# Optimization experiments

Measured on AMD Instinct MI355X. Metric: run time of the kernel, lower is better.

The kernel has to match this reference:

```python
import jax, jax.numpy as jnp
import numpy as np

N = 98304        # total nodes (= 16384 graphs * act_dim 6)
E = 1572864      # edges (avg degree 16)
C = 64           # in_channels
H = 32           # hidden_size
ACT = 6          # act_dim


def setup_inputs() -> dict:
    key = jax.random.key(0)
    ks = jax.random.split(key, 11)
    s = lambda fan: 1.0 / np.sqrt(fan)
    return {
        "state": jax.random.normal(ks[0], (N, C), jnp.float32),
        "edge_index": jax.random.randint(ks[1], (2, E), 0, N, dtype=jnp.int64),
        "conv_W": jax.random.normal(ks[2], (C, C), jnp.float32) * s(C),
        "conv_b": jax.random.normal(ks[3], (C,), jnp.float32) * 0.01,
        "W1": jax.random.normal(ks[4], (C, H), jnp.float32) * s(C),
        "b1": jax.random.normal(ks[5], (H,), jnp.float32) * 0.01,
        "W2": jax.random.normal(ks[6], (H, H), jnp.float32) * s(H),
        "b2": jax.random.normal(ks[7], (H,), jnp.float32) * 0.01,
        "W3": jax.random.normal(ks[8], (H, 1), jnp.float32) * s(H),
        "b3": jax.random.normal(ks[9], (1,), jnp.float32) * 0.01,
    }


def gcn_conv(x, edge_index, W, b):
    # PyG GCNConv: add self-loops, symmetric normalization D^-1/2 (A+I) D^-1/2 (X W) + b
    loops = jnp.arange(N, dtype=edge_index.dtype)
    src = jnp.concatenate([edge_index[0], loops])  # [E+N]
    dst = jnp.concatenate([edge_index[1], loops])  # [E+N]
    deg = jax.ops.segment_sum(jnp.ones(E + N, x.dtype), dst, num_segments=N)
    dinv = jax.lax.rsqrt(deg)                      # deg >= 1 due to self-loops
    norm = dinv[src] * dinv[dst]                   # [E+N]
    h = x @ W                                      # [N, C]
    msg = h[src] * norm[:, None]                   # gather + scale
    return jax.ops.segment_sum(msg, dst, num_segments=N) + b


def reference(state, edge_index, conv_W, conv_b, W1, b1, W2, b2, W3, b3):
    out = jax.nn.relu(gcn_conv(state, edge_index, conv_W, conv_b))
    x = out + state                                # residual
    x = x.reshape(-1, ACT, C)                      # [num_graphs, act_dim, C]
    x = jax.nn.relu(x @ W1 + b1)
    x = jax.nn.relu(x @ W2 + b2)
    x = jax.nn.softplus(x @ W3 + b3)
    concentration = x.squeeze(-1) + 1e-20          # [num_graphs, act_dim]
    return concentration
```

## Files before the change

### kernel.cpp

```cpp
#include <hip/hip_runtime.h>
#include <math.h>

#define Nn 98304
#define Ee 1572864
#define Cc 64
#define Hh 32
#define TT 128
#define NT (Nn / TT)
#define HB 256
#define EPB (Ee / HB)
#define CAPT 2560


__device__ __forceinline__ int detect64(const void* ei) {
    const unsigned int* u = (const unsigned int*)ei;
    int is64 = 1;
    #pragma unroll
    for (int i = 0; i < 16; ++i) is64 &= (u[2 * i + 1] == 0u);
    return is64;
}

__device__ __forceinline__ int load_idx(const void* ei, long e, int is64) {
    if (is64) return (int)((const long long*)ei)[e];
    return ((const int*)ei)[e];
}

__device__ __forceinline__ unsigned short f2bf(float x) {
    union { float f; unsigned int u; } v; v.f = x;
    unsigned int r = v.u + 0x7FFFu + ((v.u >> 16) & 1u);
    return (unsigned short)(r >> 16);
}
__device__ __forceinline__ float bf2f(unsigned short h) {
    union { unsigned int u; float f; } v; v.u = ((unsigned int)h) << 16;
    return v.f;
}

__global__ __launch_bounds__(1024) void k_bucket(const void* __restrict__ ei,
                                                 unsigned int* __restrict__ aux,
                                                 unsigned int* __restrict__ ebuf) {
    __shared__ unsigned int hl[NT];
    __shared__ unsigned int off[NT];
    int t = threadIdx.x, b = blockIdx.x;
    if (t < NT) hl[t] = 0;
    __syncthreads();
    int is64 = detect64(ei);
    long e0 = (long)b * EPB;
    #pragma unroll
    for (int i = 0; i < EPB / 1024; ++i) {
        int d = load_idx(ei, (long)Ee + e0 + i * 1024 + t, is64);
        atomicAdd(&hl[d >> 7], 1u);
    }
    __syncthreads();
    if (t < NT) off[t] = hl[t];
    __syncthreads();
    for (int s = 1; s < NT; s <<= 1) {
        unsigned int v = (t < NT && t >= s) ? off[t - s] : 0u;
        __syncthreads();
        if (t < NT) off[t] += v;
        __syncthreads();
    }
    if (t < NT) {
        unsigned int ex = off[t] - hl[t];
        aux[(long)b * NT + t] = ex | (hl[t] << 16);
        off[t] = ex;
    }
    __syncthreads();
    #pragma unroll
    for (int i = 0; i < EPB / 1024; ++i) {
        long e = e0 + i * 1024 + t;
        int s = load_idx(ei, e, is64);
        int d = load_idx(ei, (long)Ee + e, is64);
        unsigned int pos = atomicAdd(&off[d >> 7], 1u);
        ebuf[(long)b * EPB + pos] = (unsigned int)s | ((unsigned int)(d & (TT - 1)) << 17);
    }
}

__global__ __launch_bounds__(256) void k_nodecnt(const unsigned int* __restrict__ aux,
                                                 const unsigned int* __restrict__ ebuf,
                                                 unsigned int* __restrict__ rowOff,
                                                 unsigned int* __restrict__ rowEnd,
                                                 float* __restrict__ dinv,
                                                 unsigned int* __restrict__ srcs) {
    __shared__ unsigned int stage[CAPT];
    __shared__ unsigned int rbI[HB];
    __shared__ unsigned int ro[HB];
    __shared__ unsigned int cnt[TT];
    __shared__ unsigned int sc[TT];
    __shared__ unsigned int cur[TT];
    int t = threadIdx.x, tile = blockIdx.x;
    if (t < HB) {
        unsigned int av = aux[(long)t * NT + tile];
        ro[t] = av & 0xFFFFu;
        rbI[t] = av >> 16;
    }
    __syncthreads();
    for (int s = 1; s < HB; s <<= 1) {
        unsigned int v = (t < HB && t >= s) ? rbI[t - s] : 0u;
        __syncthreads();
        if (t < HB) rbI[t] += v;
        __syncthreads();
    }
    int total = (int)rbI[HB - 1];
    for (int i = t; i < total; i += 256) {
        int pos = 0;
        #pragma unroll
        for (int s = HB / 2; s > 0; s >>= 1)
            if ((int)rbI[pos + s - 1] <= i) pos += s;
        unsigned int prev = pos ? rbI[pos - 1] : 0u;
        stage[i] = ebuf[(long)pos * EPB + ro[pos] + (unsigned int)i - prev];
    }
    if (t < TT) cnt[t] = 0;
    __syncthreads();
    for (int i = t; i < total; i += 256)
        atomicAdd(&cnt[stage[i] >> 17], 1u);
    __syncthreads();
    if (t < TT) sc[t] = cnt[t];
    __syncthreads();
    #pragma unroll
    for (int off = 1; off < TT; off <<= 1) {
        unsigned int v = (t >= off && t < TT) ? sc[t - off] : 0u;
        __syncthreads();
        if (t < TT) sc[t] += v;
        __syncthreads();
    }
    if (t < TT) {
        unsigned int start = (unsigned int)(tile * CAPT) + sc[t] - cnt[t];
        rowOff[(long)tile * TT + t] = start;
        rowEnd[(long)tile * TT + t] = start + cnt[t];
        cur[t] = start;
        dinv[(long)tile * TT + t] = rsqrtf((float)(cnt[t] + 1));
    }
    __syncthreads();
    for (int i = t; i < total; i += 256) {
        unsigned int u = stage[i];
        unsigned int pos = atomicAdd(&cur[u >> 17], 1u);
        srcs[pos] = u & 0x1FFFFu;
    }
}

__global__ __launch_bounds__(256) void k_gemm(const float* __restrict__ state,
                                              const float* __restrict__ W,
                                              const float* __restrict__ dinv,
                                              unsigned short* __restrict__ gb) {
    __shared__ float Wl[64 * 64];
    __shared__ float Al[64 * 68];
    int t = threadIdx.x;
    long n0 = (long)blockIdx.x * 64;

    const float4* W4 = (const float4*)W;
    float4* Wl4 = (float4*)Wl;
    #pragma unroll
    for (int i = 0; i < 4; ++i) Wl4[i * 256 + t] = W4[i * 256 + t];

    const float4* S4 = (const float4*)(state) + n0 * 16;
    #pragma unroll
    for (int i = 0; i < 4; ++i) {
        int f4 = t + i * 256;
        int r = f4 >> 4, k0 = (f4 & 15) * 4;
        *(float4*)(Al + r * 68 + k0) = S4[f4];
    }
    __syncthreads();

    int r0 = (t >> 4) * 4;
    int c0 = (t & 15) * 4;
    float acc[4][4] = {{0.f}};
    #pragma unroll
    for (int kk = 0; kk < 64; kk += 4) {
        float4 a4[4], w4[4];
        #pragma unroll
        for (int i = 0; i < 4; ++i) a4[i] = *(const float4*)(Al + (r0 + i) * 68 + kk);
        #pragma unroll
        for (int j = 0; j < 4; ++j) w4[j] = *(const float4*)(Wl + (kk + j) * 64 + c0);
        const float* aa = (const float*)a4;
        const float* ww = (const float*)w4;
        #pragma unroll
        for (int i = 0; i < 4; ++i)
            #pragma unroll
            for (int j = 0; j < 4; ++j) {
                float av = aa[i * 4 + j];
                #pragma unroll
                for (int c = 0; c < 4; ++c)
                    acc[i][c] = fmaf(av, ww[j * 4 + c], acc[i][c]);
            }
    }
    #pragma unroll
    for (int i = 0; i < 4; ++i) {
        long n = n0 + r0 + i;
        float dv = dinv[n];
        ushort4 o;
        o.x = f2bf(acc[i][0] * dv); o.y = f2bf(acc[i][1] * dv);
        o.z = f2bf(acc[i][2] * dv); o.w = f2bf(acc[i][3] * dv);
        *(ushort4*)(gb + n * 64 + c0) = o;
    }
}

__global__ __launch_bounds__(256) void k_gather(const unsigned int* __restrict__ rowOff,
                                                const unsigned int* __restrict__ rowEnd,
                                                const unsigned int* __restrict__ srcs,
                                                const unsigned short* __restrict__ gb,
                                                const float* __restrict__ dinv,
                                                float* __restrict__ agg) {
    int wave = threadIdx.x >> 6, lane = threadIdx.x & 63;
    int n = blockIdx.x * 4 + wave;
    int start = (int)rowOff[n];
    int end = (int)rowEnd[n];
    float acc = bf2f(gb[(long)n * 64 + lane]);
    for (int base = start; base < end; base += 64) {
        int m = min(64, end - base);
        int sv = (lane < m) ? (int)srcs[base + lane] : 0;
        int j = 0;
        for (; j + 8 <= m; j += 8) {
            int s0 = __shfl(sv, j,     64);
            int s1 = __shfl(sv, j + 1, 64);
            int s2 = __shfl(sv, j + 2, 64);
            int s3 = __shfl(sv, j + 3, 64);
            int s4 = __shfl(sv, j + 4, 64);
            int s5 = __shfl(sv, j + 5, 64);
            int s6 = __shfl(sv, j + 6, 64);
            int s7 = __shfl(sv, j + 7, 64);
            float v0 = bf2f(gb[(long)s0 * 64 + lane]);
            float v1 = bf2f(gb[(long)s1 * 64 + lane]);
            float v2 = bf2f(gb[(long)s2 * 64 + lane]);
            float v3 = bf2f(gb[(long)s3 * 64 + lane]);
            float v4 = bf2f(gb[(long)s4 * 64 + lane]);
            float v5 = bf2f(gb[(long)s5 * 64 + lane]);
            float v6 = bf2f(gb[(long)s6 * 64 + lane]);
            float v7 = bf2f(gb[(long)s7 * 64 + lane]);
            acc += ((v0 + v1) + (v2 + v3)) + ((v4 + v5) + (v6 + v7));
        }
        for (; j + 4 <= m; j += 4) {
            int s0 = __shfl(sv, j,     64);
            int s1 = __shfl(sv, j + 1, 64);
            int s2 = __shfl(sv, j + 2, 64);
            int s3 = __shfl(sv, j + 3, 64);
            float v0 = bf2f(gb[(long)s0 * 64 + lane]);
            float v1 = bf2f(gb[(long)s1 * 64 + lane]);
            float v2 = bf2f(gb[(long)s2 * 64 + lane]);
            float v3 = bf2f(gb[(long)s3 * 64 + lane]);
            acc += (v0 + v1) + (v2 + v3);
        }
        for (; j < m; ++j) {
            int s = __shfl(sv, j, 64);
            acc += bf2f(gb[(long)s * 64 + lane]);
        }
    }
    agg[(long)n * 64 + lane] = acc * dinv[n];
}

__global__ __launch_bounds__(128) void k_final(const float* __restrict__ agg,
                                               const float* __restrict__ state,
                                               const float* __restrict__ conv_b,
                                               const float* __restrict__ W1,
                                               const float* __restrict__ b1,
                                               const float* __restrict__ W2,
                                               const float* __restrict__ b2,
                                               const float* __restrict__ W3,
                                               const float* __restrict__ b3,
                                               float* __restrict__ out) {
    __shared__ float sW1[Cc * Hh];
    __shared__ float sW2[Hh * Hh];
    __shared__ float sW3[Hh], sb1[Hh], sb2[Hh], scb[Cc];
    __shared__ float sb3;
    int t = threadIdx.x;
    for (int i = t; i < Cc * Hh; i += 128) sW1[i] = W1[i];
    for (int i = t; i < Hh * Hh; i += 128) sW2[i] = W2[i];
    if (t < Hh) { sW3[t] = W3[t]; sb1[t] = b1[t]; sb2[t] = b2[t]; }
    if (t >= 32 && t < 96) scb[t - 32] = conv_b[t - 32];
    if (t == 127) sb3 = b3[0];
    __syncthreads();

    int n = blockIdx.x * 128 + t;
    const float4* a4p = (const float4*)(agg + (long)n * 64);
    const float4* s4p = (const float4*)(state + (long)n * 64);
    float x[Cc];
    #pragma unroll
    for (int k4 = 0; k4 < 16; ++k4) {
        float4 a = a4p[k4];
        float4 s = s4p[k4];
        x[k4 * 4 + 0] = fmaxf(a.x + scb[k4 * 4 + 0], 0.f) + s.x;
        x[k4 * 4 + 1] = fmaxf(a.y + scb[k4 * 4 + 1], 0.f) + s.y;
        x[k4 * 4 + 2] = fmaxf(a.z + scb[k4 * 4 + 2], 0.f) + s.z;
        x[k4 * 4 + 3] = fmaxf(a.w + scb[k4 * 4 + 3], 0.f) + s.w;
    }
    float h1[Hh];
    #pragma unroll
    for (int j = 0; j < Hh; ++j) h1[j] = sb1[j];
    #pragma unroll
    for (int k = 0; k < Cc; ++k) {
        float xv = x[k];
        #pragma unroll
        for (int j = 0; j < Hh; ++j) h1[j] = fmaf(xv, sW1[k * Hh + j], h1[j]);
    }
    #pragma unroll
    for (int j = 0; j < Hh; ++j) h1[j] = fmaxf(h1[j], 0.f);

    float h2[Hh];
    #pragma unroll
    for (int j = 0; j < Hh; ++j) h2[j] = sb2[j];
    #pragma unroll
    for (int k = 0; k < Hh; ++k) {
        float xv = h1[k];
        #pragma unroll
        for (int j = 0; j < Hh; ++j) h2[j] = fmaf(xv, sW2[k * Hh + j], h2[j]);
    }
    float y = sb3;
    #pragma unroll
    for (int j = 0; j < Hh; ++j) y = fmaf(fmaxf(h2[j], 0.f), sW3[j], y);

    float sp = fmaxf(y, 0.f) + log1pf(expf(-fabsf(y)));
    out[n] = sp + 1e-20f;
}

extern "C" void kernel_launch(void* const* d_in, const int* in_sizes, int n_in,
                              void* d_out, int out_size, void* d_ws, size_t ws_size,
                              hipStream_t stream) {
    const float* state  = (const float*)d_in[0];
    const void*  ei     = d_in[1];
    const float* conv_W = (const float*)d_in[2];
    const float* conv_b = (const float*)d_in[3];
    const float* W1 = (const float*)d_in[4];
    const float* b1 = (const float*)d_in[5];
    const float* W2 = (const float*)d_in[6];
    const float* b2 = (const float*)d_in[7];
    const float* W3 = (const float*)d_in[8];
    const float* b3 = (const float*)d_in[9];
    float* out = (float*)d_out;

    float*          dinv   = (float*)d_ws;
    unsigned short* gb     = (unsigned short*)(dinv + Nn);
    unsigned int*   rowOff = (unsigned int*)(gb + (size_t)Nn * 64);
    unsigned int*   rowEnd = rowOff + Nn;
    unsigned int*   aux    = rowEnd + Nn;
    unsigned int*   ebuf   = aux + (size_t)HB * NT;
    unsigned int*   srcs   = ebuf + Ee;
    float*          agg    = (float*)(srcs + (size_t)NT * CAPT);

    k_bucket<<<HB, 1024, 0, stream>>>(ei, aux, ebuf);
    k_nodecnt<<<NT, 256, 0, stream>>>(aux, ebuf, rowOff, rowEnd, dinv, srcs);
    k_gemm<<<Nn / 64, 256, 0, stream>>>(state, conv_W, dinv, gb);
    k_gather<<<Nn / 4, 256, 0, stream>>>(rowOff, rowEnd, srcs, gb, dinv, agg);
    k_final<<<Nn / 128, 128, 0, stream>>>(agg, state, conv_b,
                                          W1, b1, W2, b2, W3, b3, out);
}
```

Before: 201.7 us.

## Stash dst indices in LDS, store aggregate as bf16, split gather launch

k_bucket keeps the destination indices read in its first pass in shared memory, so the second pass no longer reloads them from global memory. The gather kernel now writes its aggregate as bf16 instead of fp32, and k_final reads and unpacks that, which halves the intermediate traffic. The gather is also split into two launches, each covering half the nodes. The bf16 aggregate adds rounding error, the extra launch adds overhead, and the 24KB shared stash in k_bucket raises its LDS use.

```diff
diff --git a/kernel.cpp b/kernel.cpp
--- a/kernel.cpp
+++ b/kernel.cpp
@@ -34,12 +34,21 @@
     union { unsigned int u; float f; } v; v.u = ((unsigned int)h) << 16;
     return v.f;
 }
+__device__ __forceinline__ float bflo(unsigned int u) {
+    union { unsigned int u; float f; } v; v.u = u << 16;
+    return v.f;
+}
+__device__ __forceinline__ float bfhi(unsigned int u) {
+    union { unsigned int u; float f; } v; v.u = u & 0xFFFF0000u;
+    return v.f;
+}
 
 __global__ __launch_bounds__(1024) void k_bucket(const void* __restrict__ ei,
                                                  unsigned int* __restrict__ aux,
                                                  unsigned int* __restrict__ ebuf) {
     __shared__ unsigned int hl[NT];
     __shared__ unsigned int off[NT];
+    __shared__ unsigned int dstash[EPB];
     int t = threadIdx.x, b = blockIdx.x;
     if (t < NT) hl[t] = 0;
     __syncthreads();
@@ -48,6 +57,7 @@
     #pragma unroll
     for (int i = 0; i < EPB / 1024; ++i) {
         int d = load_idx(ei, (long)Ee + e0 + i * 1024 + t, is64);
+        dstash[i * 1024 + t] = (unsigned int)d;
         atomicAdd(&hl[d >> 7], 1u);
     }
     __syncthreads();
@@ -67,11 +77,10 @@
     __syncthreads();
     #pragma unroll
     for (int i = 0; i < EPB / 1024; ++i) {
-        long e = e0 + i * 1024 + t;
-        int s = load_idx(ei, e, is64);
-        int d = load_idx(ei, (long)Ee + e, is64);
+        int s = load_idx(ei, e0 + i * 1024 + t, is64);
+        unsigned int d = dstash[i * 1024 + t];
         unsigned int pos = atomicAdd(&off[d >> 7], 1u);
-        ebuf[(long)b * EPB + pos] = (unsigned int)s | ((unsigned int)(d & (TT - 1)) << 17);
+        ebuf[(long)b * EPB + pos] = (unsigned int)s | ((d & (TT - 1)) << 17);
     }
 }
 
@@ -199,9 +208,10 @@
                                                 const unsigned int* __restrict__ srcs,
                                                 const unsigned short* __restrict__ gb,
                                                 const float* __restrict__ dinv,
-                                                float* __restrict__ agg) {
+                                                unsigned short* __restrict__ aggb,
+                                                int nbase) {
     int wave = threadIdx.x >> 6, lane = threadIdx.x & 63;
-    int n = blockIdx.x * 4 + wave;
+    int n = nbase + blockIdx.x * 4 + wave;
     int start = (int)rowOff[n];
     int end = (int)rowEnd[n];
     float acc = bf2f(gb[(long)n * 64 + lane]);
@@ -244,10 +254,10 @@
             acc += bf2f(gb[(long)s * 64 + lane]);
         }
     }
-    agg[(long)n * 64 + lane] = acc * dinv[n];
-}
-
-__global__ __launch_bounds__(128) void k_final(const float* __restrict__ agg,
+    aggb[(long)n * 64 + lane] = f2bf(acc * dinv[n]);
+}
+
+__global__ __launch_bounds__(128) void k_final(const unsigned short* __restrict__ aggb,
                                                const float* __restrict__ state,
                                                const float* __restrict__ conv_b,
                                                const float* __restrict__ W1,
@@ -270,17 +280,22 @@
     __syncthreads();
 
     int n = blockIdx.x * 128 + t;
-    const float4* a4p = (const float4*)(agg + (long)n * 64);
+    const uint4* a4p = (const uint4*)(aggb + (long)n * 64);
     const float4* s4p = (const float4*)(state + (long)n * 64);
     float x[Cc];
     #pragma unroll
-    for (int k4 = 0; k4 < 16; ++k4) {
-        float4 a = a4p[k4];
-        float4 s = s4p[k4];
-        x[k4 * 4 + 0] = fmaxf(a.x + scb[k4 * 4 + 0], 0.f) + s.x;
-        x[k4 * 4 + 1] = fmaxf(a.y + scb[k4 * 4 + 1], 0.f) + s.y;
-        x[k4 * 4 + 2] = fmaxf(a.z + scb[k4 * 4 + 2], 0.f) + s.z;
-        x[k4 * 4 + 3] = fmaxf(a.w + scb[k4 * 4 + 3], 0.f) + s.w;
+    for (int k8 = 0; k8 < 8; ++k8) {
+        uint4 a = a4p[k8];
+        float4 s0 = s4p[2 * k8], s1 = s4p[2 * k8 + 1];
+        int k = k8 * 8;
+        x[k + 0] = fmaxf(bflo(a.x) + scb[k + 0], 0.f) + s0.x;
+        x[k + 1] = fmaxf(bfhi(a.x) + scb[k + 1], 0.f) + s0.y;
+        x[k + 2] = fmaxf(bflo(a.y) + scb[k + 2], 0.f) + s0.z;
+        x[k + 3] = fmaxf(bfhi(a.y) + scb[k + 3], 0.f) + s0.w;
+        x[k + 4] = fmaxf(bflo(a.z) + scb[k + 4], 0.f) + s1.x;
+        x[k + 5] = fmaxf(bfhi(a.z) + scb[k + 5], 0.f) + s1.y;
+        x[k + 6] = fmaxf(bflo(a.w) + scb[k + 6], 0.f) + s1.z;
+        x[k + 7] = fmaxf(bfhi(a.w) + scb[k + 7], 0.f) + s1.w;
     }
     float h1[Hh];
     #pragma unroll
@@ -333,12 +348,13 @@
     unsigned int*   aux    = rowEnd + Nn;
     unsigned int*   ebuf   = aux + (size_t)HB * NT;
     unsigned int*   srcs   = ebuf + Ee;
-    float*          agg    = (float*)(srcs + (size_t)NT * CAPT);
+    unsigned short* aggb   = (unsigned short*)(srcs + (size_t)NT * CAPT);
 
     k_bucket<<<HB, 1024, 0, stream>>>(ei, aux, ebuf);
     k_nodecnt<<<NT, 256, 0, stream>>>(aux, ebuf, rowOff, rowEnd, dinv, srcs);
     k_gemm<<<Nn / 64, 256, 0, stream>>>(state, conv_W, dinv, gb);
-    k_gather<<<Nn / 4, 256, 0, stream>>>(rowOff, rowEnd, srcs, gb, dinv, agg);
-    k_final<<<Nn / 128, 128, 0, stream>>>(agg, state, conv_b,
+    k_gather<<<Nn / 8, 256, 0, stream>>>(rowOff, rowEnd, srcs, gb, dinv, aggb, 0);
+    k_gather<<<Nn / 8, 256, 0, stream>>>(rowOff, rowEnd, srcs, gb, dinv, aggb, Nn / 2);
+    k_final<<<Nn / 128, 128, 0, stream>>>(aggb, state, conv_b,
                                           W1, b1, W2, b2, W3, b3, out);
 }
```

After: 206.3 us. 2.3% more time.
